# Performance work log

Hardware: AMD Instinct MI355X
Metric: run time of the kernel (lower is better)

Reference implementation:

```python
import jax, jax.numpy as jnp
import numpy as np

EPS = 1e-5

def layernorm(x, g, b):
    mu = jnp.mean(x, axis=-1, keepdims=True)
    var = jnp.var(x, axis=-1, keepdims=True)
    return (x - mu) * jax.lax.rsqrt(var + EPS) * g + b

def setup_inputs() -> dict:
    key = jax.random.key(0)
    ks = jax.random.split(key, 12)
    B, S, D, H, F = 2, 2048, 1024, 16, 4096
    sd = 0.02
    x = jax.random.normal(ks[0], (B, S, D), dtype=jnp.float32)
    mask = jnp.tril(jnp.ones((S, S), dtype=jnp.int32))[None, None]  # causal [1,1,S,S]
    return {
        "x": x,
        "mask": mask,
        "ln1_g": jnp.ones((D,), jnp.float32),
        "ln1_b": jnp.zeros((D,), jnp.float32),
        "Wqkv": jax.random.normal(ks[1], (D, 3 * D), jnp.float32) * sd,
        "bqkv": jnp.zeros((3 * D,), jnp.float32),
        "Wo": jax.random.normal(ks[2], (D, D), jnp.float32) * sd,
        "bo": jnp.zeros((D,), jnp.float32),
        "ln2_g": jnp.ones((D,), jnp.float32),
        "ln2_b": jnp.zeros((D,), jnp.float32),
        "W1": jax.random.normal(ks[3], (D, F), jnp.float32) * sd,
        "b1": jnp.zeros((F,), jnp.float32),
        "W2": jax.random.normal(ks[4], (F, D), jnp.float32) * sd,
        "b2": jnp.zeros((D,), jnp.float32),
    }

def reference(x, mask, ln1_g, ln1_b, Wqkv, bqkv, Wo, bo, ln2_g, ln2_b, W1, b1, W2, b2):
    B, S, D = x.shape
    H = 16
    hd = D // H
    scale = hd ** -0.5
    # --- attention sublayer (pre-LN) ---
    h = layernorm(x, ln1_g, ln1_b)
    qkv = h @ Wqkv + bqkv                             # [B,S,3D]
    qkv = qkv.reshape(B, S, 3, H, hd)
    q = jnp.transpose(qkv[:, :, 0], (0, 2, 1, 3))      # [B,H,S,hd]
    k = jnp.transpose(qkv[:, :, 1], (0, 2, 1, 3))
    v = jnp.transpose(qkv[:, :, 2], (0, 2, 1, 3))
    scores = jnp.einsum('bhqd,bhkd->bhqk', q, k) * scale
    scores = jnp.where(mask == 0, -jnp.inf, scores)
    attn = jax.nn.softmax(scores, axis=-1)
    out = jnp.einsum('bhqk,bhkd->bhqd', attn, v)
    out = jnp.transpose(out, (0, 2, 1, 3)).reshape(B, S, D)
    x = x + (out @ Wo + bo)
    # --- FFN sublayer (pre-LN) ---
    h = layernorm(x, ln2_g, ln2_b)
    h = jax.nn.gelu(h @ W1 + b1, approximate=False)
    x = x + (h @ W2 + b2)
    return x
```

## Files before the change

kernel.cpp:

```cpp
#include <hip/hip_runtime.h>

typedef __bf16 bf16x8 __attribute__((ext_vector_type(8)));
typedef float f32x4 __attribute__((ext_vector_type(4)));

typedef const void __attribute__((address_space(1))) gvoid_t;
typedef void __attribute__((address_space(3))) lvoid_t;

__device__ __forceinline__ void gload16(const void* g, void* l) {
  __builtin_amdgcn_global_load_lds((gvoid_t*)g, (lvoid_t*)l, 16, 0, 0);
}

__device__ __forceinline__ unsigned short f2b(float f) {
  unsigned int u = __builtin_bit_cast(unsigned int, f);
  u = (u + 0x7FFFu + ((u >> 16) & 1u)) >> 16;
  return (unsigned short)u;
}

__device__ __forceinline__ unsigned cvt_pk_bf16(float lo, float hi) {
  unsigned r;
  asm("v_cvt_pk_bf16_f32 %0, %1, %2" : "=v"(r) : "v"(lo), "v"(hi));
  return r;
}

__global__ __launch_bounds__(256) void ln_kernel(
    const float* __restrict__ x, const float* __restrict__ g,
    const float* __restrict__ b, unsigned short* __restrict__ out) {
  const int row = blockIdx.x;
  const int t = threadIdx.x;
  const float4 v = *(const float4*)(x + (size_t)row * 1024 + t * 4);
  float s1 = v.x + v.y + v.z + v.w;
  float s2 = v.x * v.x + v.y * v.y + v.z * v.z + v.w * v.w;
#pragma unroll
  for (int off = 32; off > 0; off >>= 1) {
    s1 += __shfl_down(s1, off, 64);
    s2 += __shfl_down(s2, off, 64);
  }
  __shared__ float red[8];
  const int wid = t >> 6;
  if ((t & 63) == 0) { red[wid] = s1; red[wid + 4] = s2; }
  __syncthreads();
  s1 = red[0] + red[1] + red[2] + red[3];
  s2 = red[4] + red[5] + red[6] + red[7];
  const float mu = s1 * (1.0f / 1024.0f);
  const float var = s2 * (1.0f / 1024.0f) - mu * mu;
  const float rs = rsqrtf(var + 1e-5f);
  const float4 gv = *(const float4*)(g + t * 4);
  const float4 bv = *(const float4*)(b + t * 4);
  ushort4 o;
  o.x = f2b((v.x - mu) * rs * gv.x + bv.x);
  o.y = f2b((v.y - mu) * rs * gv.y + bv.y);
  o.z = f2b((v.z - mu) * rs * gv.z + bv.z);
  o.w = f2b((v.w - mu) * rs * gv.w + bv.w);
  *(ushort4*)(out + (size_t)row * 1024 + t * 4) = o;
}

__global__ __launch_bounds__(256) void prep_kernel(
    const float* __restrict__ x, const float* __restrict__ ln1_g,
    const float* __restrict__ ln1_b,
    const float* __restrict__ Wqkv, const float* __restrict__ Wo,
    const float* __restrict__ W1, const float* __restrict__ W2,
    unsigned short* __restrict__ bWqkv, unsigned short* __restrict__ bWo,
    unsigned short* __restrict__ bW1, unsigned short* __restrict__ bW2,
    unsigned short* __restrict__ h) {
  __shared__ float tl[32][33];
  __shared__ float red[8];
  const int flat = blockIdx.x;
  const int t = threadIdx.x;
  if (flat >= 12288) {
    const int row = flat - 12288;
    const float4 v = *(const float4*)(x + (size_t)row * 1024 + t * 4);
    float s1 = v.x + v.y + v.z + v.w;
    float s2 = v.x * v.x + v.y * v.y + v.z * v.z + v.w * v.w;
#pragma unroll
    for (int off = 32; off > 0; off >>= 1) {
      s1 += __shfl_down(s1, off, 64);
      s2 += __shfl_down(s2, off, 64);
    }
    const int wid = t >> 6;
    if ((t & 63) == 0) { red[wid] = s1; red[wid + 4] = s2; }
    __syncthreads();
    s1 = red[0] + red[1] + red[2] + red[3];
    s2 = red[4] + red[5] + red[6] + red[7];
    const float mu = s1 * (1.0f / 1024.0f);
    const float var = s2 * (1.0f / 1024.0f) - mu * mu;
    const float rs = rsqrtf(var + 1e-5f);
    const float4 gv = *(const float4*)(ln1_g + t * 4);
    const float4 bv = *(const float4*)(ln1_b + t * 4);
    ushort4 o;
    o.x = f2b((v.x - mu) * rs * gv.x + bv.x);
    o.y = f2b((v.y - mu) * rs * gv.y + bv.y);
    o.z = f2b((v.z - mu) * rs * gv.z + bv.z);
    o.w = f2b((v.w - mu) * rs * gv.w + bv.w);
    *(ushort4*)(h + (size_t)row * 1024 + t * 4) = o;
    return;
  }
  const float* W;
  unsigned short* Wt;
  int K, N, nx, f;
  if (flat < 3072)      { W = Wqkv; Wt = bWqkv; K = 1024; N = 3072; nx = 96;  f = flat; }
  else if (flat < 4096) { W = Wo;   Wt = bWo;   K = 1024; N = 1024; nx = 32;  f = flat - 3072; }
  else if (flat < 8192) { W = W1;   Wt = bW1;   K = 1024; N = 4096; nx = 128; f = flat - 4096; }
  else                  { W = W2;   Wt = bW2;   K = 4096; N = 1024; nx = 32;  f = flat - 8192; }
  const int n0 = (f % nx) * 32, k0 = (f / nx) * 32;
  const int tx = t & 31, ty = t >> 5;
#pragma unroll
  for (int i = 0; i < 4; ++i) {
    int k = ty + i * 8;
    tl[k][tx] = W[(size_t)(k0 + k) * N + n0 + tx];
  }
  __syncthreads();
#pragma unroll
  for (int i = 0; i < 4; ++i) {
    int n = ty + i * 8;
    Wt[(size_t)(n0 + n) * K + k0 + tx] = f2b(tl[tx][n]);
  }
}

template <int EPI>
__global__ __launch_bounds__(256) void gemm_kernel(
    const unsigned short* __restrict__ A, const unsigned short* __restrict__ Bt,
    const float* __restrict__ bias, const float* __restrict__ resid,
    float* __restrict__ Cf, unsigned short* __restrict__ Cb,
    int M, int N, int K) {
  __shared__ __align__(16) char lds[98304];
  const int tid = threadIdx.x;
  const int lane = tid & 63, w = tid >> 6;
  const int wr = w >> 1, wc = w & 1;
  const int bm0 = blockIdx.x * 128, bn0 = blockIdx.y * 128;

  f32x4 acc[4][4] = {};

  const int rr = lane >> 3;
  const int slog = (lane & 7) ^ rr;
  const unsigned short* gA = A + (size_t)(bm0 + w * 32 + rr) * K + slog * 8;
  const unsigned short* gB = Bt + (size_t)(bn0 + w * 32 + rr) * K + slog * 8;
  const size_t rstep8 = (size_t)8 * K;

  const int l15 = lane & 15;
  const int g = lane >> 4;

  const int nt = K >> 6;

  auto STAGE = [&](int t, int buf) {
    const int k0 = t << 6;
    char* ab = lds + buf * 32768 + w * 4096;
    char* bb = lds + buf * 32768 + 16384 + w * 4096;
#pragma unroll
    for (int j = 0; j < 4; ++j) {
      gload16(gA + j * rstep8 + k0, ab + j * 1024);
      gload16(gB + j * rstep8 + k0, bb + j * 1024);
    }
  };

  STAGE(0, 0);
  STAGE(1 < nt ? 1 : 0, 1);
  int cur = 0;

  for (int t = 0; t < nt; ++t) {
    asm volatile("s_waitcnt vmcnt(8)" ::: "memory");
    __builtin_amdgcn_sched_barrier(0);
    __builtin_amdgcn_s_barrier();
    __builtin_amdgcn_sched_barrier(0);

    const char* ldsA = lds + cur * 32768;
    const char* ldsB = ldsA + 16384;
#pragma unroll
    for (int kk = 0; kk < 2; ++kk) {
      bf16x8 af[4], bfr[4];
#pragma unroll
      for (int m = 0; m < 4; ++m) {
        const int tr = wr * 64 + m * 16 + l15;
        af[m] = *(const bf16x8*)(ldsA + tr * 128 + (((kk * 4 + g) ^ (tr & 7)) << 4));
      }
#pragma unroll
      for (int n = 0; n < 4; ++n) {
        const int tc = wc * 64 + n * 16 + l15;
        bfr[n] = *(const bf16x8*)(ldsB + tc * 128 + (((kk * 4 + g) ^ (tc & 7)) << 4));
      }
      __builtin_amdgcn_s_setprio(1);
#pragma unroll
      for (int m = 0; m < 4; ++m)
#pragma unroll
        for (int n = 0; n < 4; ++n)
          acc[m][n] =
              __builtin_amdgcn_mfma_f32_16x16x32_bf16(af[m], bfr[n], acc[m][n], 0, 0, 0);
      __builtin_amdgcn_s_setprio(0);
    }

    __builtin_amdgcn_sched_barrier(0);
    const int t2 = (t + 2 < nt) ? t + 2 : nt - 1;
    STAGE(t2, cur ? cur - 1 : 2);
    cur = (cur == 2) ? 0 : cur + 1;
  }

#pragma unroll
  for (int mm = 0; mm < 4; ++mm) {
    const int r0 = bm0 + wr * 64 + mm * 16 + (g << 2);
#pragma unroll
    for (int nn = 0; nn < 4; ++nn) {
      const int c = bn0 + wc * 64 + nn * 16 + l15;
      const float bv = bias[c];
#pragma unroll
      for (int i = 0; i < 4; ++i) {
        const size_t idx = (size_t)(r0 + i) * N + c;
        float v = acc[mm][nn][i] + bv;
        if constexpr (EPI == 1) {
          v += resid[idx];
          Cf[idx] = v;
        } else if constexpr (EPI == 2) {
          v = 0.5f * v * (1.0f + erff(v * 0.70710678118654752f));
          Cb[idx] = f2b(v);
        } else if constexpr (EPI == 3) {
          Cb[idx] = f2b(v);
        } else {
          Cf[idx] = v;
        }
      }
    }
  }
}

template <int EPI>
__global__ __launch_bounds__(512) void gemm8w_kernel(
    const unsigned short* __restrict__ A, const unsigned short* __restrict__ Bt,
    const float* __restrict__ bias, const float* __restrict__ resid,
    float* __restrict__ Cf, unsigned short* __restrict__ Cb,
    unsigned short* __restrict__ vtp,
    int M, int N, int K) {
  __shared__ __align__(16) char lds[73728];
  const int tid = threadIdx.x;
  const int lane = tid & 63, w = tid >> 6;
  const int wr = w >> 1, wc = w & 1;
  const int bm0 = blockIdx.x * 256, bn0 = blockIdx.y * 128;

  f32x4 acc[4][4] = {};

  const int gcol = (lane & 3) ^ ((lane >> 3) & 3);
  const unsigned short* gA =
      A + (size_t)(bm0 + w * 32 + (lane >> 2)) * K + gcol * 8;
  const unsigned short* gB =
      Bt + (size_t)(bn0 + w * 16 + (lane >> 2)) * K + gcol * 8;
  const size_t rstep = (size_t)16 * K;

  const int l15 = lane & 15;
  const int g = lane >> 4;

  const int nt = K >> 5;

  auto STAGE = [&](int t, int buf) {
    const int k0 = t << 5;
    char* base = lds + buf * 24576;
    gload16(gA + k0, base + w * 2048);
    gload16(gA + rstep + k0, base + w * 2048 + 1024);
    gload16(gB + k0, base + 16384 + w * 1024);
  };

  STAGE(0, 0);
  STAGE(1 < nt ? 1 : 0, 1);
  int cur = 0;

  for (int t = 0; t < nt; ++t) {
    asm volatile("s_waitcnt vmcnt(3)" ::: "memory");
    __builtin_amdgcn_sched_barrier(0);
    __builtin_amdgcn_s_barrier();
    __builtin_amdgcn_sched_barrier(0);

    const char* ldsA = lds + cur * 24576;
    const char* ldsB = ldsA + 16384;
    bf16x8 af[4], bfr[4];
#pragma unroll
    for (int m = 0; m < 4; ++m) {
      const int tr = wr * 64 + m * 16 + l15;
      const int slot = g ^ ((tr >> 1) & 3);
      af[m] = *(const bf16x8*)(ldsA + tr * 64 + slot * 16);
    }
#pragma unroll
    for (int n = 0; n < 4; ++n) {
      const int tc = wc * 64 + n * 16 + l15;
      const int slot = g ^ ((tc >> 1) & 3);
      bfr[n] = *(const bf16x8*)(ldsB + tc * 64 + slot * 16);
    }
    __builtin_amdgcn_s_setprio(1);
#pragma unroll
    for (int m = 0; m < 4; ++m)
#pragma unroll
      for (int n = 0; n < 4; ++n)
        acc[m][n] =
            __builtin_amdgcn_mfma_f32_16x16x32_bf16(af[m], bfr[n], acc[m][n], 0, 0, 0);
    __builtin_amdgcn_s_setprio(0);

    __builtin_amdgcn_sched_barrier(0);
    const int t2 = (t + 2 < nt) ? t + 2 : nt - 1;
    STAGE(t2, cur ? cur - 1 : 2);
    cur = (cur == 2) ? 0 : cur + 1;
  }

#pragma unroll
  for (int mm = 0; mm < 4; ++mm) {
    const int r0 = bm0 + wr * 64 + mm * 16 + (g << 2);
#pragma unroll
    for (int nn = 0; nn < 4; ++nn) {
      const int c = bn0 + wc * 64 + nn * 16 + l15;
      const float bv = bias[c];
#pragma unroll
      for (int i = 0; i < 4; ++i) {
        const size_t idx = (size_t)(r0 + i) * N + c;
        float v = acc[mm][nn][i] + bv;
        if constexpr (EPI == 1) {
          v += resid[idx];
          Cf[idx] = v;
        } else if constexpr (EPI == 2) {
          v = 0.5f * v * (1.0f + erff(v * 0.70710678118654752f));
          Cb[idx] = f2b(v);
        } else if constexpr (EPI == 3) {
          const unsigned short bvs = f2b(v);
          if (c < 2048) {
            Cb[idx] = bvs;
          } else {
            const int row = r0 + i;
            const int d = c - 2048;
            vtp[((size_t)((row >> 11) * 16 + (d >> 6)) * 64 + (d & 63)) * 2048 +
                (row & 2047)] = bvs;
          }
        } else {
          Cf[idx] = v;
        }
      }
    }
  }
}

__global__ __launch_bounds__(512) void attn_mfma_kernel(
    const unsigned short* __restrict__ qkv, const unsigned short* __restrict__ vt,
    unsigned short* __restrict__ out) {
  __shared__ __align__(16) char Kl[24576];
  __shared__ __align__(16) char Vl[24576];
  __shared__ __align__(16) char Pl[16384];
  const int bh = blockIdx.x;
  const int b = bh >> 4, h = bh & 15;
  const int qtile = (int)gridDim.y - 1 - (int)blockIdx.y;
  const int q0 = qtile * 128;
  const int tid = threadIdx.x;
  const int lane = tid & 63, w = tid >> 6;
  const int l15 = lane & 15, g = lane >> 4;
  const size_t rowbase = (size_t)b * 2048;
  const float SC2 = 0.18033688011112042f;

  bf16x8 aq[2];
  {
    const unsigned short* qp = qkv + (rowbase + q0 + w * 16 + l15) * 3072 + h * 64 + g * 8;
    aq[0] = __builtin_bit_cast(bf16x8, *(const uint4*)qp);
    aq[1] = __builtin_bit_cast(bf16x8, *(const uint4*)(qp + 32));
  }

  f32x4 oacc[4] = {};
  float lrow[4] = {0.f, 0.f, 0.f, 0.f};

  const int srow = w * 8 + (lane >> 3);
  const int slog = (lane & 7) ^ (lane >> 3);
  const unsigned short* kS = qkv + (rowbase + srow) * 3072 + 1024 + h * 64 + slog * 8;
  const unsigned short* vS = vt + ((size_t)bh * 64 + srow) * 2048 + slog * 8;
  const int nt = 2 * qtile + 2;

  auto STAGE = [&](int t, int buf) {
    const int kb = t * 64;
    gload16(kS + (size_t)kb * 3072, Kl + buf * 8192 + w * 1024);
    gload16(vS + kb, Vl + buf * 8192 + w * 1024);
  };

  STAGE(0, 0);
  STAGE(1 < nt ? 1 : 0, 1);
  int cur = 0;

  for (int kt = 0; kt < nt; ++kt) {
    const int kb = kt * 64;
    asm volatile("s_waitcnt vmcnt(2)" ::: "memory");
    __builtin_amdgcn_sched_barrier(0);
    __builtin_amdgcn_s_barrier();
    __builtin_amdgcn_sched_barrier(0);

    const char* Kc = Kl + cur * 8192;
    const char* Vc = Vl + cur * 8192;

    f32x4 sacc[4] = {};
    __builtin_amdgcn_s_setprio(1);
#pragma unroll
    for (int kk = 0; kk < 2; ++kk) {
#pragma unroll
      for (int n = 0; n < 4; ++n) {
        const int r = n * 16 + l15;
        bf16x8 bk = *(const bf16x8*)(Kc + r * 128 + (((kk * 4 + g) ^ (r & 7)) << 4));
        sacc[n] = __builtin_amdgcn_mfma_f32_16x16x32_bf16(aq[kk], bk, sacc[n], 0, 0, 0);
      }
    }
    __builtin_amdgcn_s_setprio(0);

    const bool diag = (kb + 63 > q0 + w * 16);
    float p[4][4];
#pragma unroll
    for (int i = 0; i < 4; ++i) {
      const int qrel = q0 + w * 16 + g * 4 + i - kb;
      float ls = 0.f;
#pragma unroll
      for (int n = 0; n < 4; ++n) {
        float pv = __builtin_amdgcn_exp2f(sacc[n][i] * SC2);
        if (diag && (l15 + 16 * n > qrel)) pv = 0.f;
        p[n][i] = pv;
        ls += pv;
      }
      lrow[i] += ls;
    }

#pragma unroll
    for (int n = 0; n < 4; ++n) {
      const int col = l15 + 16 * n;
#pragma unroll
      for (int i = 0; i < 4; i += 2) {
        const unsigned pk = cvt_pk_bf16(p[n][i], p[n][i + 1]);
        const int r0b = g * 4 + i, r1b = g * 4 + i + 1;
        *(unsigned short*)(Pl + w * 2048 + ((r0b * 128 + col * 2) ^ ((r0b & 7) << 4))) =
            (unsigned short)pk;
        *(unsigned short*)(Pl + w * 2048 + ((r1b * 128 + col * 2) ^ ((r1b & 7) << 4))) =
            (unsigned short)(pk >> 16);
      }
    }
#pragma unroll
    for (int kk = 0; kk < 2; ++kk) {
      bf16x8 ap = *(const bf16x8*)(Pl + w * 2048 + ((l15 * 128 + g * 16 + kk * 64) ^ ((l15 & 7) << 4)));
      __builtin_amdgcn_s_setprio(1);
#pragma unroll
      for (int dn = 0; dn < 4; ++dn) {
        const int r = dn * 16 + l15;
        bf16x8 bv = *(const bf16x8*)(Vc + r * 128 + (((kk * 4 + g) ^ (r & 7)) << 4));
        oacc[dn] = __builtin_amdgcn_mfma_f32_16x16x32_bf16(ap, bv, oacc[dn], 0, 0, 0);
      }
      __builtin_amdgcn_s_setprio(0);
    }

    __builtin_amdgcn_sched_barrier(0);
    const int t2 = (kt + 2 < nt) ? kt + 2 : nt - 1;
    STAGE(t2, cur ? cur - 1 : 2);
    cur = (cur == 2) ? 0 : cur + 1;
  }

#pragma unroll
  for (int i = 0; i < 4; ++i) {
    float l = lrow[i];
#pragma unroll
    for (int off = 8; off >= 1; off >>= 1) l += __shfl_xor(l, off, 64);
    const float inv = 1.0f / l;
    unsigned short* op = out + (rowbase + q0 + w * 16 + g * 4 + i) * 1024 + h * 64 + l15;
#pragma unroll
    for (int dn = 0; dn < 4; ++dn) op[dn * 16] = f2b(oacc[dn][i] * inv);
  }
}

extern "C" void kernel_launch(void* const* d_in, const int* in_sizes, int n_in,
                              void* d_out, int out_size, void* d_ws, size_t ws_size,
                              hipStream_t stream) {
  const float* x = (const float*)d_in[0];
  const float* ln1_g = (const float*)d_in[2];
  const float* ln1_b = (const float*)d_in[3];
  const float* Wqkv = (const float*)d_in[4];
  const float* bqkv = (const float*)d_in[5];
  const float* Wo = (const float*)d_in[6];
  const float* bo = (const float*)d_in[7];
  const float* ln2_g = (const float*)d_in[8];
  const float* ln2_b = (const float*)d_in[9];
  const float* W1 = (const float*)d_in[10];
  const float* b1 = (const float*)d_in[11];
  const float* W2 = (const float*)d_in[12];
  const float* b2 = (const float*)d_in[13];
  float* outp = (float*)d_out;

  const int M = 4096, D = 1024, F = 4096;
  char* ws = (char*)d_ws;
  size_t o = 0;
  auto alloc = [&](size_t bytes) {
    size_t r = o;
    o += (bytes + 255) & ~(size_t)255;
    return r;
  };
  unsigned short* bWqkv = (unsigned short*)(ws + alloc((size_t)3072 * D * 2));
  unsigned short* bWo   = (unsigned short*)(ws + alloc((size_t)D * D * 2));
  unsigned short* bW1   = (unsigned short*)(ws + alloc((size_t)F * D * 2));
  unsigned short* bW2   = (unsigned short*)(ws + alloc((size_t)D * F * 2));
  unsigned short* h     = (unsigned short*)(ws + alloc((size_t)M * D * 2));
  unsigned short* qkvb  = (unsigned short*)(ws + alloc((size_t)M * F * 2));
  unsigned short* attn  = (unsigned short*)(ws + alloc((size_t)M * D * 2));
  float* x1             = (float*)(ws + alloc((size_t)M * D * 4));
  unsigned short* vt    = (unsigned short*)(ws + alloc((size_t)32 * 64 * 2048 * 2));
  unsigned short* f1 = qkvb;
  unsigned short* h2 = h;

  prep_kernel<<<16384, 256, 0, stream>>>(x, ln1_g, ln1_b, Wqkv, Wo, W1, W2,
                                         bWqkv, bWo, bW1, bW2, h);
  gemm8w_kernel<3><<<dim3(M / 256, 3072 / 128), 512, 0, stream>>>(
      h, bWqkv, bqkv, nullptr, nullptr, qkvb, vt, M, 3072, D);
  attn_mfma_kernel<<<dim3(32, 16), 512, 0, stream>>>(qkvb, vt, attn);
  gemm_kernel<1><<<dim3(M / 128, D / 128), 256, 0, stream>>>(
      attn, bWo, bo, x, x1, nullptr, M, D, D);
  ln_kernel<<<M, 256, 0, stream>>>(x1, ln2_g, ln2_b, h2);
  gemm8w_kernel<2><<<dim3(M / 256, F / 128), 512, 0, stream>>>(
      h2, bW1, b1, nullptr, nullptr, f1, nullptr, M, F, D);
  gemm_kernel<1><<<dim3(M / 128, D / 128), 256, 0, stream>>>(
      f1, bW2, b2, x1, outp, nullptr, M, D, F);
}
```

Baseline: 216.2 us.

## Add 256x256 ping-pong pipelined GEMM kernel for the FFN up-projection

Adds a new bf16 MFMA GEMM kernel with 256x256 block tiles and 128KB of double-buffered LDS. It splits each K-tile into four quadrant MFMA phases, interleaving direct global-to-LDS loads with barriers, wait counts and raised priority around the MFMA clusters. The FFN W1 GEMM with GELU epilogue now uses it instead of the 256x128 kernel. The aim is to raise data reuse per tile and to hide load latency behind matrix work. The cost is half as many blocks (256 on the GPU), heavy LDS use that limits each CU to one block, and a tight hand-written schedule that is fragile.

```diff
diff --git a/kernel.cpp b/kernel.cpp
--- a/kernel.cpp
+++ b/kernel.cpp
@@ -330,6 +330,141 @@
   }
 }
 
+template <int EPI>
+__global__ __launch_bounds__(512) void gemm8p_kernel(
+    const unsigned short* __restrict__ A, const unsigned short* __restrict__ Bt,
+    const float* __restrict__ bias,
+    float* __restrict__ Cf, unsigned short* __restrict__ Cb,
+    int M, int N, int K) {
+  __shared__ __align__(16) char lds[131072];
+  const int tid = threadIdx.x;
+  const int lane = tid & 63, w = tid >> 6;
+  const int wr = w >> 2, wc = w & 3;
+  const int l15 = lane & 15, g = lane >> 4;
+  const int bm0 = blockIdx.x * 256, bn0 = blockIdx.y * 256;
+
+  f32x4 acc[2][2][4][2] = {};
+  bf16x8 af[4][2], bf0[2][2], bf1[2][2];
+
+  const int slog = (lane & 7) ^ (lane >> 3);
+  const unsigned short* gA = A + (size_t)(bm0 + w * 8 + (lane >> 3)) * K + slog * 8;
+  const unsigned short* gB = Bt + (size_t)(bn0 + w * 8 + (lane >> 3)) * K + slog * 8;
+  const size_t r64 = (size_t)64 * K;
+  const size_t r128 = (size_t)128 * K;
+
+  auto SA = [&](int t, int b, int h) {
+    const unsigned short* s = gA + h * r128 + (t << 6);
+    char* d = lds + b * 65536 + h * 16384 + w * 1024;
+    gload16(s, d);
+    gload16(s + r64, d + 8192);
+  };
+  auto SB = [&](int t, int b, int h) {
+    const unsigned short* s = gB + h * r128 + (t << 6);
+    char* d = lds + b * 65536 + 32768 + h * 16384 + w * 1024;
+    gload16(s, d);
+    gload16(s + r64, d + 8192);
+  };
+
+#define RD_A(BASE, MH)                                                       \
+  _Pragma("unroll") for (int m = 0; m < 4; ++m)                              \
+  _Pragma("unroll") for (int kk = 0; kk < 2; ++kk) {                         \
+    const int r = wr * 64 + m * 16 + l15;                                    \
+    af[m][kk] = *(const bf16x8*)((BASE) + (MH) * 16384 + r * 128 +           \
+                                 (((kk * 4 + g) ^ (r & 7)) << 4));           \
+  }
+#define RD_B(BASE, NH, DST)                                                  \
+  _Pragma("unroll") for (int n = 0; n < 2; ++n)                              \
+  _Pragma("unroll") for (int kk = 0; kk < 2; ++kk) {                         \
+    const int r = wc * 32 + n * 16 + l15;                                    \
+    DST[n][kk] = *(const bf16x8*)((BASE) + 32768 + (NH) * 16384 + r * 128 +  \
+                                  (((kk * 4 + g) ^ (r & 7)) << 4));          \
+  }
+#define MFMA_Q(MH, NH, BF)                                                   \
+  __builtin_amdgcn_s_setprio(1);                                             \
+  _Pragma("unroll") for (int m = 0; m < 4; ++m)                              \
+  _Pragma("unroll") for (int n = 0; n < 2; ++n)                              \
+  _Pragma("unroll") for (int kk = 0; kk < 2; ++kk)                           \
+      acc[MH][NH][m][n] = __builtin_amdgcn_mfma_f32_16x16x32_bf16(           \
+          af[m][kk], BF[n][kk], acc[MH][NH][m][n], 0, 0, 0);                 \
+  __builtin_amdgcn_s_setprio(0);
+#define BAR_IN                                                               \
+  __builtin_amdgcn_sched_barrier(0);                                         \
+  __builtin_amdgcn_s_barrier();                                              \
+  asm volatile("s_waitcnt lgkmcnt(0)" ::: "memory");                         \
+  __builtin_amdgcn_sched_barrier(0);
+#define BAR_OUT                                                              \
+  __builtin_amdgcn_sched_barrier(0);                                         \
+  __builtin_amdgcn_s_barrier();                                              \
+  __builtin_amdgcn_sched_barrier(0);
+#define VMC6                                                                 \
+  asm volatile("s_waitcnt vmcnt(6)" ::: "memory");                           \
+  __builtin_amdgcn_sched_barrier(0);
+
+  const int nkt = K >> 6;
+  const char* B0p = lds;
+  const char* B1p = lds + 65536;
+
+  SA(0, 0, 0); SB(0, 0, 0); SB(0, 0, 1); SA(0, 0, 1);
+  SA(1, 1, 0); SB(1, 1, 0); SB(1, 1, 1);
+  VMC6;
+  __builtin_amdgcn_s_barrier();
+  __builtin_amdgcn_sched_barrier(0);
+
+  const int niter = nkt >> 1;
+  for (int i = 0; i < niter; ++i) {
+    const int t1 = 2 * i + 1;
+    const int c2 = (2 * i + 2 < nkt) ? 2 * i + 2 : nkt - 1;
+    const int c3 = (2 * i + 3 < nkt) ? 2 * i + 3 : nkt - 1;
+    RD_A(B0p, 0); RD_B(B0p, 0, bf0); SA(t1, 1, 1);
+    BAR_IN; MFMA_Q(0, 0, bf0); BAR_OUT;
+    RD_B(B0p, 1, bf1); SA(c2, 0, 0);
+    BAR_IN; MFMA_Q(0, 1, bf1); BAR_OUT;
+    RD_A(B0p, 1); SB(c2, 0, 0);
+    BAR_IN; MFMA_Q(1, 0, bf0); BAR_OUT;
+    SB(c2, 0, 1);
+    VMC6; BAR_IN; MFMA_Q(1, 1, bf1); BAR_OUT;
+    RD_A(B1p, 0); RD_B(B1p, 0, bf0); SA(c2, 0, 1);
+    BAR_IN; MFMA_Q(0, 0, bf0); BAR_OUT;
+    RD_B(B1p, 1, bf1); SA(c3, 1, 0);
+    BAR_IN; MFMA_Q(0, 1, bf1); BAR_OUT;
+    RD_A(B1p, 1); SB(c3, 1, 0);
+    BAR_IN; MFMA_Q(1, 0, bf0); BAR_OUT;
+    SB(c3, 1, 1);
+    VMC6; BAR_IN; MFMA_Q(1, 1, bf1); BAR_OUT;
+  }
+
+#pragma unroll
+  for (int mh = 0; mh < 2; ++mh)
+#pragma unroll
+    for (int mm = 0; mm < 4; ++mm) {
+      const int r0 = bm0 + mh * 128 + wr * 64 + mm * 16 + (g << 2);
+#pragma unroll
+      for (int nh = 0; nh < 2; ++nh)
+#pragma unroll
+        for (int nn = 0; nn < 2; ++nn) {
+          const int c = bn0 + nh * 128 + wc * 32 + nn * 16 + l15;
+          const float bv = bias[c];
+#pragma unroll
+          for (int i = 0; i < 4; ++i) {
+            const size_t idx = (size_t)(r0 + i) * N + c;
+            float v = acc[mh][nh][mm][nn][i] + bv;
+            if constexpr (EPI == 2) {
+              v = 0.5f * v * (1.0f + erff(v * 0.70710678118654752f));
+              Cb[idx] = f2b(v);
+            } else {
+              Cf[idx] = v;
+            }
+          }
+        }
+    }
+#undef RD_A
+#undef RD_B
+#undef MFMA_Q
+#undef BAR_IN
+#undef BAR_OUT
+#undef VMC6
+}
+
 __global__ __launch_bounds__(512) void attn_mfma_kernel(
     const unsigned short* __restrict__ qkv, const unsigned short* __restrict__ vt,
     unsigned short* __restrict__ out) {
@@ -501,8 +636,8 @@
   gemm_kernel<1><<<dim3(M / 128, D / 128), 256, 0, stream>>>(
       attn, bWo, bo, x, x1, nullptr, M, D, D);
   ln_kernel<<<M, 256, 0, stream>>>(x1, ln2_g, ln2_b, h2);
-  gemm8w_kernel<2><<<dim3(M / 256, F / 128), 512, 0, stream>>>(
-      h2, bW1, b1, nullptr, nullptr, f1, nullptr, M, F, D);
+  gemm8p_kernel<2><<<dim3(M / 256, F / 256), 512, 0, stream>>>(
+      h2, bW1, b1, nullptr, f1, M, F, D);
   gemm_kernel<1><<<dim3(M / 128, D / 128), 256, 0, stream>>>(
       f1, bW2, b2, x1, outp, nullptr, M, D, F);
 }
```

Measured after the change: 218.0 us. No clear change (+0.8%).
